# Performance work log

Hardware: AMD Instinct MI355X
Metric: run time of the kernel (lower is better)

## Reference

```python
import jax, jax.numpy as jnp
import numpy as np

N, M, D = 4096, 4096, 16


def setup_inputs() -> dict:
    key = jax.random.key(0)
    k1, k2, k3, k4 = jax.random.split(key, 4)
    x = jax.random.normal(k1, (N, D), dtype=jnp.float32)
    xx = jax.random.normal(k2, (M, D), dtype=jnp.float32)
    # free-form (pre-softplus) kernel parameters
    scale_ff = jax.random.uniform(k3, (D,), dtype=jnp.float32)
    variance_ff = jax.random.uniform(k4, (), dtype=jnp.float32)
    return {"x": x, "xx": xx, "scale_ff": scale_ff, "variance_ff": variance_ff}


def reference(x, xx, scale_ff, variance_ff):
    # positive() in AutoForce is softplus (free_form is its inverse)
    scale = jax.nn.softplus(scale_ff)          # [D]
    variance = jax.nn.softplus(variance_ff)    # scalar (diag amplitude)
    # r: [N, M, D] pairwise scaled differences (the large broadcast intermediate)
    r = (x[:, None, :] - xx[None, :, :]) / scale
    # K = exp(-||r||^2 / 2) * variance, shape [N, M]
    cov = jnp.exp(-0.5 * jnp.sum(r * r, axis=-1)) * variance
    return cov
```

## Files before the change

### kernel.cpp

```cpp
#include <hip/hip_runtime.h>
#include <math.h>


#define NN 4096
#define MM 4096
#define DD 16
#define RS 20

__global__ __launch_bounds__(256, 4)
void rbf_kernel(const float* __restrict__ x, const float* __restrict__ xx,
                const float* __restrict__ scale_ff,
                const float* __restrict__ variance_ff,
                float* __restrict__ out) {
  __shared__ __align__(16) float s_inv[DD];
  __shared__ float s_lnvar;
  __shared__ __align__(16) float s_a[64 * RS];

  const int tid  = threadIdx.x;
  const int lane = tid & 63;
  const int wave = tid >> 6;

  const int i0 = blockIdx.y * 64;
  const int j0 = blockIdx.x * 256;

  if (tid < DD) {
    s_inv[tid] = 1.0f / log1pf(expf(scale_ff[tid]));
  }
  if (tid == DD) {
    s_lnvar = logf(log1pf(expf(variance_ff[0])));
  }
  __syncthreads();

  {
    const int row = tid >> 2;
    const int c   = tid & 3;
    float4 xv = *(const float4*)&x[(i0 + row) * DD + c * 4];
    float4 iv = *(const float4*)&s_inv[c * 4];
    xv.x *= iv.x; xv.y *= iv.y; xv.z *= iv.z; xv.w *= iv.w;
    *(float4*)&s_a[row * RS + c * 4] = xv;
  }
  __syncthreads();

  if (tid < 64) {
    float s = 0.f;
#pragma unroll
    for (int c = 0; c < 4; ++c) {
      float4 v = *(const float4*)&s_a[tid * RS + c * 4];
      s = fmaf(v.x, v.x, s); s = fmaf(v.y, v.y, s);
      s = fmaf(v.z, v.z, s); s = fmaf(v.w, v.w, s);
    }
    s_a[tid * RS + DD] = 0.5f * s - s_lnvar;
  }

  float4 b[4][4];
  float dn[4];
  {
    float4 iv[4];
#pragma unroll
    for (int c = 0; c < 4; ++c) iv[c] = *(const float4*)&s_inv[c * 4];
    const int jb = j0 + (lane << 2);
#pragma unroll
    for (int r = 0; r < 4; ++r) {
      float s = 0.f;
#pragma unroll
      for (int c = 0; c < 4; ++c) {
        float4 v = *(const float4*)&xx[(size_t)(jb + r) * DD + c * 4];
        v.x *= iv[c].x; v.y *= iv[c].y; v.z *= iv[c].z; v.w *= iv[c].w;
        b[r][c] = v;
        s = fmaf(v.x, v.x, s); s = fmaf(v.y, v.y, s);
        s = fmaf(v.z, v.z, s); s = fmaf(v.w, v.w, s);
      }
      dn[r] = 0.5f * s;
    }
  }

  __syncthreads();

  const int jb = j0 + (lane << 2);

#pragma unroll 2
  for (int ii = 0; ii < 16; ++ii) {
    const int li = wave * 16 + ii;
    const float* ap = &s_a[li * RS];
    const float4 a0 = *(const float4*)&ap[0];
    const float4 a1 = *(const float4*)&ap[4];
    const float4 a2 = *(const float4*)&ap[8];
    const float4 a3 = *(const float4*)&ap[12];
    const float cc  = ap[DD];

    float acc[4] = {0.f, 0.f, 0.f, 0.f};
#pragma unroll
    for (int r = 0; r < 4; ++r) {
      float s = 0.f;
      s = fmaf(a0.x, b[r][0].x, s); s = fmaf(a0.y, b[r][0].y, s);
      s = fmaf(a0.z, b[r][0].z, s); s = fmaf(a0.w, b[r][0].w, s);
      s = fmaf(a1.x, b[r][1].x, s); s = fmaf(a1.y, b[r][1].y, s);
      s = fmaf(a1.z, b[r][1].z, s); s = fmaf(a1.w, b[r][1].w, s);
      s = fmaf(a2.x, b[r][2].x, s); s = fmaf(a2.y, b[r][2].y, s);
      s = fmaf(a2.z, b[r][2].z, s); s = fmaf(a2.w, b[r][2].w, s);
      s = fmaf(a3.x, b[r][3].x, s); s = fmaf(a3.y, b[r][3].y, s);
      s = fmaf(a3.z, b[r][3].z, s); s = fmaf(a3.w, b[r][3].w, s);
      acc[r] = s;
    }

    float4 o;
    o.x = __expf(acc[0] - cc - dn[0]);
    o.y = __expf(acc[1] - cc - dn[1]);
    o.z = __expf(acc[2] - cc - dn[2]);
    o.w = __expf(acc[3] - cc - dn[3]);
    *(float4*)&out[(size_t)(i0 + li) * MM + jb] = o;
  }
}

extern "C" void kernel_launch(void* const* d_in, const int* in_sizes, int n_in,
                              void* d_out, int out_size, void* d_ws, size_t ws_size,
                              hipStream_t stream) {
  const float* x   = (const float*)d_in[0];
  const float* xx  = (const float*)d_in[1];
  const float* sc  = (const float*)d_in[2];
  const float* var = (const float*)d_in[3];
  float* out = (float*)d_out;

  dim3 grid(MM / 256, NN / 64);
  dim3 block(256);
  rbf_kernel<<<grid, block, 0, stream>>>(x, xx, sc, var, out);
}
```

Before: 89.11 us.

## Retile to 16 rows by 1024 columns, fold log2e into operands, use exp2

Changes the block tile from 64x256 to 16x1024, so each wave handles its own 256-column slice over the same 16 rows. The x rows are now read straight from global memory (broadcast across the wave) instead of being staged in LDS. log2(e) is folded into the scaled xx operands and the bias terms, so the inner loop accumulates from a precomputed bias and finishes with a raw v_exp (exp2) with no extra subtractions. The ii loop is fully unrolled. The tradeoff is that the x tile is reused across fewer columns per xx load, and the loop relies on uniform global loads; the kernel is mostly limited by the output write bandwidth anyway.

```diff
diff --git a/kernel.cpp b/kernel.cpp
--- a/kernel.cpp
+++ b/kernel.cpp
@@ -5,7 +5,8 @@
 #define NN 4096
 #define MM 4096
 #define DD 16
-#define RS 20
+#define L2E 1.44269504f
+#define HL2E 0.72134752f
 
 __global__ __launch_bounds__(256, 4)
 void rbf_kernel(const float* __restrict__ x, const float* __restrict__ xx,
@@ -13,85 +14,91 @@
                 const float* __restrict__ variance_ff,
                 float* __restrict__ out) {
   __shared__ __align__(16) float s_inv[DD];
-  __shared__ float s_lnvar;
-  __shared__ __align__(16) float s_a[64 * RS];
+  __shared__ __align__(16) float s_il[DD];
+  __shared__ float s_lnvarL;
+  __shared__ float s_cc[16];
 
   const int tid  = threadIdx.x;
   const int lane = tid & 63;
   const int wave = tid >> 6;
 
-  const int i0 = blockIdx.y * 64;
-  const int j0 = blockIdx.x * 256;
+  const int i0 = blockIdx.y * 16;
+  const int j0 = blockIdx.x * 1024;
 
   if (tid < DD) {
-    s_inv[tid] = 1.0f / log1pf(expf(scale_ff[tid]));
+    const float sp  = log1pf(expf(scale_ff[tid]));
+    const float inv = 1.0f / sp;
+    s_inv[tid] = inv;
+    s_il[tid]  = inv * L2E;
   }
   if (tid == DD) {
-    s_lnvar = logf(log1pf(expf(variance_ff[0])));
+    s_lnvarL = L2E * logf(log1pf(expf(variance_ff[0])));
   }
   __syncthreads();
 
-  {
-    const int row = tid >> 2;
-    const int c   = tid & 3;
-    float4 xv = *(const float4*)&x[(i0 + row) * DD + c * 4];
-    float4 iv = *(const float4*)&s_inv[c * 4];
-    xv.x *= iv.x; xv.y *= iv.y; xv.z *= iv.z; xv.w *= iv.w;
-    *(float4*)&s_a[row * RS + c * 4] = xv;
-  }
-  __syncthreads();
-
-  if (tid < 64) {
+  if (tid < 16) {
     float s = 0.f;
+    const float* xp = x + (size_t)(i0 + tid) * DD;
 #pragma unroll
     for (int c = 0; c < 4; ++c) {
-      float4 v = *(const float4*)&s_a[tid * RS + c * 4];
-      s = fmaf(v.x, v.x, s); s = fmaf(v.y, v.y, s);
-      s = fmaf(v.z, v.z, s); s = fmaf(v.w, v.w, s);
+      const float4 v  = *(const float4*)(xp + 4 * c);
+      const float4 iv = *(const float4*)&s_inv[4 * c];
+      const float ax = v.x * iv.x, ay = v.y * iv.y;
+      const float az = v.z * iv.z, aw = v.w * iv.w;
+      s = fmaf(ax, ax, s); s = fmaf(ay, ay, s);
+      s = fmaf(az, az, s); s = fmaf(aw, aw, s);
     }
-    s_a[tid * RS + DD] = 0.5f * s - s_lnvar;
+    s_cc[tid] = fmaf(HL2E, s, -s_lnvarL);
   }
 
   float4 b[4][4];
-  float dn[4];
+  float ndn[4];
   {
-    float4 iv[4];
+    float4 iv[4], il[4];
 #pragma unroll
-    for (int c = 0; c < 4; ++c) iv[c] = *(const float4*)&s_inv[c * 4];
-    const int jb = j0 + (lane << 2);
+    for (int c = 0; c < 4; ++c) {
+      iv[c] = *(const float4*)&s_inv[4 * c];
+      il[c] = *(const float4*)&s_il[4 * c];
+    }
+    const int jb = j0 + (wave << 8) + (lane << 2);
 #pragma unroll
     for (int r = 0; r < 4; ++r) {
       float s = 0.f;
 #pragma unroll
       for (int c = 0; c < 4; ++c) {
-        float4 v = *(const float4*)&xx[(size_t)(jb + r) * DD + c * 4];
-        v.x *= iv[c].x; v.y *= iv[c].y; v.z *= iv[c].z; v.w *= iv[c].w;
-        b[r][c] = v;
-        s = fmaf(v.x, v.x, s); s = fmaf(v.y, v.y, s);
-        s = fmaf(v.z, v.z, s); s = fmaf(v.w, v.w, s);
+        const float4 v = *(const float4*)&xx[(size_t)(jb + r) * DD + 4 * c];
+        const float tx = v.x * iv[c].x, ty = v.y * iv[c].y;
+        const float tz = v.z * iv[c].z, tw = v.w * iv[c].w;
+        s = fmaf(tx, tx, s); s = fmaf(ty, ty, s);
+        s = fmaf(tz, tz, s); s = fmaf(tw, tw, s);
+        b[r][c].x = tx * il[c].x; b[r][c].y = ty * il[c].y;
+        b[r][c].z = tz * il[c].z; b[r][c].w = tw * il[c].w;
       }
-      dn[r] = 0.5f * s;
+      ndn[r] = -HL2E * s;
     }
   }
 
   __syncthreads();
 
-  const int jb = j0 + (lane << 2);
+  const int jb = j0 + (wave << 8) + (lane << 2);
+  const float* __restrict__ xw = x + (size_t)i0 * DD;
+  float* __restrict__ op = out + (size_t)i0 * MM + jb;
 
-#pragma unroll 2
+#pragma unroll
   for (int ii = 0; ii < 16; ++ii) {
-    const int li = wave * 16 + ii;
-    const float* ap = &s_a[li * RS];
-    const float4 a0 = *(const float4*)&ap[0];
-    const float4 a1 = *(const float4*)&ap[4];
-    const float4 a2 = *(const float4*)&ap[8];
-    const float4 a3 = *(const float4*)&ap[12];
-    const float cc  = ap[DD];
+    const float4 a0 = *(const float4*)(xw + ii * DD + 0);
+    const float4 a1 = *(const float4*)(xw + ii * DD + 4);
+    const float4 a2 = *(const float4*)(xw + ii * DD + 8);
+    const float4 a3 = *(const float4*)(xw + ii * DD + 12);
+    const float cc  = s_cc[ii];
 
-    float acc[4] = {0.f, 0.f, 0.f, 0.f};
+    float acc[4];
+#pragma unroll
+    for (int r = 0; r < 4; ++r) acc[r] = ndn[r] - cc;
+
 #pragma unroll
     for (int r = 0; r < 4; ++r) {
-      float s = 0.f;
+      float s = acc[r];
       s = fmaf(a0.x, b[r][0].x, s); s = fmaf(a0.y, b[r][0].y, s);
       s = fmaf(a0.z, b[r][0].z, s); s = fmaf(a0.w, b[r][0].w, s);
       s = fmaf(a1.x, b[r][1].x, s); s = fmaf(a1.y, b[r][1].y, s);
@@ -99,16 +106,16 @@
       s = fmaf(a2.x, b[r][2].x, s); s = fmaf(a2.y, b[r][2].y, s);
       s = fmaf(a2.z, b[r][2].z, s); s = fmaf(a2.w, b[r][2].w, s);
       s = fmaf(a3.x, b[r][3].x, s); s = fmaf(a3.y, b[r][3].y, s);
-      s = fmaf(a3.z, b[r][3].z, s); s = fmaf(a3.w, b[r][3].w, s);
+      s = fmaf(a3.w, b[r][3].w, s); s = fmaf(a3.z, b[r][3].z, s);
       acc[r] = s;
     }
 
     float4 o;
-    o.x = __expf(acc[0] - cc - dn[0]);
-    o.y = __expf(acc[1] - cc - dn[1]);
-    o.z = __expf(acc[2] - cc - dn[2]);
-    o.w = __expf(acc[3] - cc - dn[3]);
-    *(float4*)&out[(size_t)(i0 + li) * MM + jb] = o;
+    o.x = __builtin_amdgcn_exp2f(acc[0]);
+    o.y = __builtin_amdgcn_exp2f(acc[1]);
+    o.z = __builtin_amdgcn_exp2f(acc[2]);
+    o.w = __builtin_amdgcn_exp2f(acc[3]);
+    *(float4*)(op + (size_t)ii * MM) = o;
   }
 }
 
@@ -121,7 +128,7 @@
   const float* var = (const float*)d_in[3];
   float* out = (float*)d_out;
 
-  dim3 grid(MM / 256, NN / 64);
+  dim3 grid(MM / 1024, NN / 16);
   dim3 block(256);
   rbf_kernel<<<grid, block, 0, stream>>>(x, xx, sc, var, out);
 }
```

Result: slower. 93.82 us (+5.3%).
